# Kernel optimization log

Measured on AMD Instinct MI355X. Metric: run time of the kernel, lower is better.

## Reference

```python
import jax, jax.numpy as jnp
import numpy as np

B, C, H, W = 16, 128, 48, 48
C4 = C // 4
N = H * W
BN_EPS = 1e-5


def conv_bn_relu(x, w, gamma, beta, mean, var):
    # 1x1 conv (no bias) as channel contraction, then eval-mode BatchNorm, then ReLU
    y = jnp.einsum('bchw,oc->bohw', x, w)
    scale = gamma / jnp.sqrt(var + BN_EPS)
    y = y * scale[None, :, None, None] + (beta - mean * scale)[None, :, None, None]
    return jax.nn.relu(y)


def setup_inputs() -> dict:
    key = jax.random.key(0)
    ks = jax.random.split(key, 16)
    inp = {
        'x_en': jax.random.normal(ks[0], (B, C, H, W), dtype=jnp.float32),
        'x_de': jax.random.normal(ks[1], (B, C, H, W), dtype=jnp.float32),
        'x_cat': jax.random.normal(ks[2], (B, 2 * C, H, W), dtype=jnp.float32),
        # Get_KQ: Conv2d(C -> C/4, 1x1, no bias) + BN(C/4) (shared for K and Q)
        'w_kq': jax.random.normal(ks[3], (C4, C), dtype=jnp.float32) * 0.05,
        'kq_gamma': jax.random.normal(ks[4], (C4,), dtype=jnp.float32) * 0.1 + 1.0,
        'kq_beta': jax.random.normal(ks[5], (C4,), dtype=jnp.float32) * 0.1,
        'kq_mean': jax.random.normal(ks[6], (C4,), dtype=jnp.float32) * 0.1,
        'kq_var': jax.random.uniform(ks[7], (C4,), dtype=jnp.float32) + 0.5,
        # Get_V: Conv2d(C -> C, 1x1, no bias) + BN(C)
        'w_v': jax.random.normal(ks[8], (C, C), dtype=jnp.float32) * 0.05,
        'v_gamma': jax.random.normal(ks[9], (C,), dtype=jnp.float32) * 0.1 + 1.0,
        'v_beta': jax.random.normal(ks[10], (C,), dtype=jnp.float32) * 0.1,
        'v_mean': jax.random.normal(ks[11], (C,), dtype=jnp.float32) * 0.1,
        'v_var': jax.random.uniform(ks[12], (C,), dtype=jnp.float32) + 0.5,
        # reduce_channels: Conv2d(2C -> C, 1x1, no bias) + BN(C)
        'w_red': jax.random.normal(ks[13], (C, 2 * C), dtype=jnp.float32) * 0.05,
        'red_gamma': jax.random.normal(ks[14], (C,), dtype=jnp.float32) * 0.1 + 1.0,
        'red_beta': jax.random.normal(ks[15], (C,), dtype=jnp.float32) * 0.1,
        'red_mean': jax.random.normal(jax.random.fold_in(key, 100), (C,), dtype=jnp.float32) * 0.1,
        'red_var': jax.random.uniform(jax.random.fold_in(key, 101), (C,), dtype=jnp.float32) + 0.5,
    }
    return inp


def reference(x_en, x_de, x_cat,
              w_kq, kq_gamma, kq_beta, kq_mean, kq_var,
              w_v, v_gamma, v_beta, v_mean, v_var,
              w_red, red_gamma, red_beta, red_mean, red_var):
    Kf = conv_bn_relu(x_en, w_kq, kq_gamma, kq_beta, kq_mean, kq_var).reshape(B, C4, N)
    Qf = conv_bn_relu(x_de, w_kq, kq_gamma, kq_beta, kq_mean, kq_var).reshape(B, C4, N)
    # KQ[b, n, m] = sum_k K[b, k, n] * Q[b, k, m]  -> [B, N, N]
    KQ = jnp.einsum('bkn,bkm->bnm', Kf, Qf)
    # GLOBAL softmax over the flattened N*N map (per batch), not per row
    A = jax.nn.softmax(KQ.reshape(B, N * N), axis=1).reshape(B, N, N)
    x = conv_bn_relu(x_cat, w_red, red_gamma, red_beta, red_mean, red_var)
    V = conv_bn_relu(x, w_v, v_gamma, v_beta, v_mean, v_var).reshape(B, C, N)
    # FeatureMap[b, c, n] = sum_m V[b, c, m] * A[b, n, m]
    feat = jnp.einsum('bcm,bnm->bcn', V, A).reshape(B, C, H, W)
    return jnp.concatenate([x, feat], axis=1)
```

## Files before the change

### kernel.cpp

```cpp
#include <hip/hip_runtime.h>
#include <math.h>

#define C    128
#define C4   32
#define NN   2304
#define BN_EPS 1e-5f
#define NEG_INF -3.402823466e38f
#define LOG2E 1.4426950408889634f

typedef short bf16x8 __attribute__((ext_vector_type(8)));
typedef float f32x4 __attribute__((ext_vector_type(4)));

#define SOFT_BARRIER() asm volatile("s_waitcnt lgkmcnt(0)\n\ts_barrier" ::: "memory")

__device__ inline unsigned short f2bf(float f) {
    unsigned int u = __float_as_uint(f);
    u += 0x7fffu + ((u >> 16) & 1u);
    return (unsigned short)(u >> 16);
}

__device__ inline unsigned int pk2bf(float a, float b) {
#if __has_builtin(__builtin_amdgcn_cvt_pk_bf16_f32)
    typedef __bf16 bf2 __attribute__((ext_vector_type(2)));
    bf2 v = __builtin_amdgcn_cvt_pk_bf16_f32(a, b);
    return __builtin_bit_cast(unsigned int, v);
#else
    unsigned int ua = __float_as_uint(a); ua += 0x7fffu + ((ua >> 16) & 1u);
    unsigned int ub = __float_as_uint(b); ub += 0x7fffu + ((ub >> 16) & 1u);
    return __builtin_amdgcn_perm(ub, ua, 0x07060302u);
#endif
}

__device__ inline float fexp2(float x) {
#if __has_builtin(__builtin_amdgcn_exp2f)
    return __builtin_amdgcn_exp2f(x);
#else
    return __expf(x * 0.69314718055994531f);
#endif
}


__global__ __launch_bounds__(256) void k_wprep(
    const float* __restrict__ wkq, const float* __restrict__ kq_g,
    const float* __restrict__ kq_b, const float* __restrict__ kq_m,
    const float* __restrict__ kq_v,
    const float* __restrict__ wv, const float* __restrict__ v_g,
    const float* __restrict__ v_b, const float* __restrict__ v_m,
    const float* __restrict__ v_v,
    const float* __restrict__ wred, const float* __restrict__ red_g,
    const float* __restrict__ red_b, const float* __restrict__ red_m,
    const float* __restrict__ red_v,
    unsigned short* __restrict__ wkq_bf, unsigned short* __restrict__ wv_bf,
    unsigned short* __restrict__ wred_bf,
    float* __restrict__ kq_sh, float* __restrict__ v_sh, float* __restrict__ red_sh)
{
    const int t = blockIdx.x * 256 + threadIdx.x;
    if (t < 4096) {
        const int o = t >> 7;
        const float sc = kq_g[o] * rsqrtf(kq_v[o] + BN_EPS);
        wkq_bf[t] = f2bf(wkq[t] * sc);
        if ((t & 127) == 0) kq_sh[o] = kq_b[o] - kq_m[o] * sc;
    } else if (t < 4096 + 16384) {
        const int e = t - 4096;
        const int o = e >> 7;
        const float sc = v_g[o] * rsqrtf(v_v[o] + BN_EPS);
        wv_bf[e] = f2bf(wv[e] * sc);
        if ((e & 127) == 0) v_sh[o] = v_b[o] - v_m[o] * sc;
    } else if (t < 4096 + 16384 + 32768) {
        const int e = t - 20480;
        const int o = e >> 8;
        const float sc = red_g[o] * rsqrtf(red_v[o] + BN_EPS);
        wred_bf[e] = f2bf(wred[e] * sc);
        if ((e & 255) == 0) red_sh[o] = red_b[o] - red_m[o] * sc;
    }
}

__global__ __launch_bounds__(256) void k_kq(
    const float* __restrict__ x0, const float* __restrict__ x1,
    const unsigned short* __restrict__ wbf, const float* __restrict__ shift,
    unsigned short* __restrict__ Kt, unsigned short* __restrict__ Qt)
{
    constexpr int NTILE = 128, R = 8;
    __shared__ unsigned short Xs[NTILE][40];

    const int tid = threadIdx.x;
    const int w = tid >> 6, lane = tid & 63;
    const int quad = lane >> 4, l16 = lane & 15;
    const int b = blockIdx.y, n0 = blockIdx.x * NTILE;
    const int nbase = w * 32;

    const float* xin = (blockIdx.z ? x1 : x0) + (size_t)b * C * NN;
    const int p = tid & 15, g = tid >> 4;

    f32x4 acc[2][2];
#pragma unroll
    for (int mt = 0; mt < 2; mt++)
#pragma unroll
        for (int nt = 0; nt < 2; nt++) acc[mt][nt] = (f32x4){0.f, 0.f, 0.f, 0.f};

    for (int c0 = 0; c0 < C; c0 += 32) {
        __syncthreads();
        {
            const float* xr = xin + (size_t)(c0 + 2 * p) * NN + n0 + g * R;
            float av[R], bv[R];
#pragma unroll
            for (int i4 = 0; i4 < R; i4 += 4) {
                *(float4*)&av[i4] = *(const float4*)&xr[i4];
                *(float4*)&bv[i4] = *(const float4*)&xr[NN + i4];
            }
            unsigned int* Xw = (unsigned int*)Xs;
#pragma unroll
            for (int i = 0; i < R; i++)
                Xw[(g * R + i) * 20 + p] = pk2bf(av[i], bv[i]);
        }
        __syncthreads();
        bf16x8 af[2];
#pragma unroll
        for (int mt = 0; mt < 2; mt++)
            af[mt] = *(const bf16x8*)&wbf[(size_t)(mt * 16 + l16) * C + c0 + quad * 8];
#pragma unroll
        for (int nt = 0; nt < 2; nt++) {
            const bf16x8 bfr = *(const bf16x8*)&Xs[nbase + nt * 16 + l16][quad * 8];
#pragma unroll
            for (int mt = 0; mt < 2; mt++)
                acc[mt][nt] = __builtin_amdgcn_mfma_f32_16x16x32_bf16(af[mt], bfr, acc[mt][nt], 0, 0, 0);
        }
    }

    unsigned short* ob16 = blockIdx.z ? Qt : Kt;
    const float osc = blockIdx.z ? 1.f : LOG2E;
#pragma unroll
    for (int mt = 0; mt < 2; mt++)
#pragma unroll
        for (int nt = 0; nt < 2; nt++)
#pragma unroll
            for (int r = 0; r < 4; r++) {
                const int o = mt * 16 + quad * 4 + r;
                const int n = n0 + nbase + nt * 16 + l16;
                const float sh = shift[o];
                ob16[((size_t)b * NN + n) * 32 + o] =
                    f2bf(fmaxf(acc[mt][nt][r] + sh, 0.f) * osc);
            }
}

__global__ __launch_bounds__(256) void k_redv(
    const float* __restrict__ xcat,
    const unsigned short* __restrict__ wred_bf, const float* __restrict__ red_sh,
    const unsigned short* __restrict__ wv_bf,  const float* __restrict__ v_sh,
    float* __restrict__ out, unsigned short* __restrict__ Vf)
{
    __shared__ unsigned short Xs[64][40];
    __shared__ unsigned int   Xv[64 * 65];

    const int tid = threadIdx.x;
    const int w = tid >> 6, lane = tid & 63;
    const int quad = lane >> 4, l16 = lane & 15;
    const int b = blockIdx.y, n0 = blockIdx.x * 64;
    const float* xin = xcat + (size_t)b * 2 * C * NN;
    const int p = tid & 15, g = tid >> 4;

    f32x4 acc[2][4];
#pragma unroll
    for (int mt = 0; mt < 2; mt++)
#pragma unroll
        for (int nt = 0; nt < 4; nt++) acc[mt][nt] = (f32x4){0.f, 0.f, 0.f, 0.f};

    for (int c0 = 0; c0 < 2 * C; c0 += 32) {
        __syncthreads();
        {
            const float* xr = xin + (size_t)(c0 + 2 * p) * NN + n0 + g * 4;
            float4 av = *(const float4*)&xr[0];
            float4 bv = *(const float4*)&xr[NN];
            unsigned int* Xw = (unsigned int*)Xs;
            Xw[(g * 4 + 0) * 20 + p] = pk2bf(av.x, bv.x);
            Xw[(g * 4 + 1) * 20 + p] = pk2bf(av.y, bv.y);
            Xw[(g * 4 + 2) * 20 + p] = pk2bf(av.z, bv.z);
            Xw[(g * 4 + 3) * 20 + p] = pk2bf(av.w, bv.w);
        }
        __syncthreads();
        bf16x8 af[2];
#pragma unroll
        for (int mt = 0; mt < 2; mt++)
            af[mt] = *(const bf16x8*)&wred_bf[(size_t)(w * 32 + mt * 16 + l16) * (2 * C) + c0 + quad * 8];
#pragma unroll
        for (int nt = 0; nt < 4; nt++) {
            const bf16x8 bfr = *(const bf16x8*)&Xs[nt * 16 + l16][quad * 8];
#pragma unroll
            for (int mt = 0; mt < 2; mt++)
                acc[mt][nt] = __builtin_amdgcn_mfma_f32_16x16x32_bf16(af[mt], bfr, acc[mt][nt], 0, 0, 0);
        }
    }

    {
        float* ob = out + (size_t)b * (2 * C * NN);
#pragma unroll
        for (int mt = 0; mt < 2; mt++) {
            float sh[4];
#pragma unroll
            for (int r = 0; r < 4; r++) sh[r] = red_sh[w * 32 + mt * 16 + quad * 4 + r];
#pragma unroll
            for (int nt = 0; nt < 4; nt++) {
                const int n = n0 + nt * 16 + l16;
                float v[4];
#pragma unroll
                for (int r = 0; r < 4; r++) {
                    const int o = w * 32 + mt * 16 + quad * 4 + r;
                    v[r] = fmaxf(acc[mt][nt][r] + sh[r], 0.f);
                    ob[(size_t)o * NN + n] = v[r];
                }
                const int op0 = 16 * w + mt * 8 + quad * 2;
                Xv[(op0 + 0) * 65 + nt * 16 + l16] = pk2bf(v[0], v[1]);
                Xv[(op0 + 1) * 65 + nt * 16 + l16] = pk2bf(v[2], v[3]);
            }
        }
    }
    SOFT_BARRIER();

    f32x4 vacc[2][4];
#pragma unroll
    for (int mt = 0; mt < 2; mt++)
#pragma unroll
        for (int nt = 0; nt < 4; nt++) vacc[mt][nt] = (f32x4){0.f, 0.f, 0.f, 0.f};

    for (int c0 = 0; c0 < C; c0 += 32) {
        bf16x8 af[2];
#pragma unroll
        for (int mt = 0; mt < 2; mt++)
            af[mt] = *(const bf16x8*)&wv_bf[(size_t)(w * 32 + mt * 16 + l16) * C + c0 + quad * 8];
#pragma unroll
        for (int nt = 0; nt < 4; nt++) {
            const int col = nt * 16 + l16;
            const int cp0 = c0 / 2 + quad * 4;
            uint4 u;
            u.x = Xv[(cp0 + 0) * 65 + col];
            u.y = Xv[(cp0 + 1) * 65 + col];
            u.z = Xv[(cp0 + 2) * 65 + col];
            u.w = Xv[(cp0 + 3) * 65 + col];
            const bf16x8 bfr = __builtin_bit_cast(bf16x8, u);
#pragma unroll
            for (int mt = 0; mt < 2; mt++)
                vacc[mt][nt] = __builtin_amdgcn_mfma_f32_16x16x32_bf16(af[mt], bfr, vacc[mt][nt], 0, 0, 0);
        }
    }

#pragma unroll
    for (int mt = 0; mt < 2; mt++) {
        float sh[4];
#pragma unroll
        for (int r = 0; r < 4; r++) sh[r] = v_sh[w * 32 + mt * 16 + quad * 4 + r];
#pragma unroll
        for (int nt = 0; nt < 4; nt++)
#pragma unroll
            for (int r = 0; r < 4; r++) {
                const int o = w * 32 + mt * 16 + quad * 4 + r;
                const int n = n0 + nt * 16 + l16;
                Vf[((size_t)b * C + o) * NN + n] = f2bf(fmaxf(vacc[mt][nt][r] + sh[r], 0.f));
            }
    }
}

__global__ __launch_bounds__(256) void k_stats(
    const unsigned short* __restrict__ Kt, const unsigned short* __restrict__ Qt,
    float* __restrict__ bmax, float* __restrict__ bsum)
{
    const int tid = threadIdx.x;
    const int w = tid >> 6, lane = tid & 63;
    const int quad = lane >> 4, l16 = lane & 15;
    const int b = blockIdx.z;
    const int n0 = blockIdx.x * 128, m0 = blockIdx.y * 128;
    const unsigned short* Kb = Kt + (size_t)b * NN * 32;
    const unsigned short* Qb = Qt + (size_t)b * NN * 32;

    bf16x8 kf[8], qf[2];
#pragma unroll
    for (int nt = 0; nt < 8; nt++)
        kf[nt] = *(const bf16x8*)&Kb[(size_t)(n0 + nt * 16 + l16) * 32 + quad * 8];
#pragma unroll
    for (int mt = 0; mt < 2; mt++)
        qf[mt] = *(const bf16x8*)&Qb[(size_t)(m0 + w * 32 + mt * 16 + l16) * 32 + quad * 8];

    f32x4 s[16];
#pragma unroll
    for (int mt = 0; mt < 2; mt++)
#pragma unroll
        for (int nt = 0; nt < 8; nt++) {
            f32x4 z = (f32x4){0.f, 0.f, 0.f, 0.f};
            s[mt * 8 + nt] = __builtin_amdgcn_mfma_f32_16x16x32_bf16(qf[mt], kf[nt], z, 0, 0, 0);
        }

    float lmax = NEG_INF;
#pragma unroll
    for (int i = 0; i < 16; i++)
        lmax = fmaxf(lmax, fmaxf(fmaxf(s[i][0], s[i][1]), fmaxf(s[i][2], s[i][3])));
    float lsum = 0.f;
#pragma unroll
    for (int i = 0; i < 16; i++)
        lsum += fexp2(s[i][0] - lmax) + fexp2(s[i][1] - lmax) +
                fexp2(s[i][2] - lmax) + fexp2(s[i][3] - lmax);

#pragma unroll
    for (int off = 32; off > 0; off >>= 1) {
        const float omax = __shfl_xor(lmax, off);
        const float osum = __shfl_xor(lsum, off);
        const float nmax = fmaxf(lmax, omax);
        lsum = lsum * fexp2(lmax - nmax) + osum * fexp2(omax - nmax);
        lmax = nmax;
    }
    __shared__ float smax[4], ssum[4];
    if (lane == 0) { smax[w] = lmax; ssum[w] = lsum; }
    __syncthreads();
    if (tid == 0) {
        float M = smax[0], S = ssum[0];
        for (int i = 1; i < 4; i++) {
            const float nmax = fmaxf(M, smax[i]);
            S = S * fexp2(M - nmax) + ssum[i] * fexp2(smax[i] - nmax);
            M = nmax;
        }
        const int idx = (b * 18 + blockIdx.y) * 18 + blockIdx.x;
        bmax[idx] = M;
        bsum[idx] = S;
    }
}

__global__ __launch_bounds__(256) void k_fin(
    const float* __restrict__ bmax, const float* __restrict__ bsum,
    float* __restrict__ Ms, float* __restrict__ Sinv)
{
    __shared__ float rmax[256], rsum[256];
    const int b = blockIdx.x, tid = threadIdx.x;
    float lmax = NEG_INF, lsum = 0.f;
    for (int i = tid; i < 324; i += 256) {
        const float m = bmax[b * 324 + i], s = bsum[b * 324 + i];
        const float nmax = fmaxf(lmax, m);
        lsum = lsum * fexp2(lmax - nmax) + s * fexp2(m - nmax);
        lmax = nmax;
    }
    rmax[tid] = lmax; rsum[tid] = lsum;
    __syncthreads();
    for (int st = 128; st > 0; st >>= 1) {
        if (tid < st) {
            const float m2 = rmax[tid + st], s2 = rsum[tid + st];
            const float nmax = fmaxf(rmax[tid], m2);
            rsum[tid] = rsum[tid] * fexp2(rmax[tid] - nmax) + s2 * fexp2(m2 - nmax);
            rmax[tid] = nmax;
        }
        __syncthreads();
    }
    if (tid == 0) { Ms[b] = rmax[0]; Sinv[b] = 1.f / rsum[0]; }
}

__global__ __launch_bounds__(256) void k_feat(
    const unsigned short* __restrict__ Kt, const unsigned short* __restrict__ Qt,
    const unsigned short* __restrict__ Vf, const float* __restrict__ Ms,
    const float* __restrict__ Sinv, float* __restrict__ out)
{
    __shared__ __align__(16) unsigned short Et[64][72];
    const int tid = threadIdx.x;
    const int w = tid >> 6, lane = tid & 63;
    const int quad = lane >> 4, l16 = lane & 15;
    const int b = blockIdx.y, n0 = blockIdx.x * 64;
    const unsigned short* Kb = Kt + (size_t)b * NN * 32;
    const unsigned short* Qb = Qt + (size_t)b * NN * 32;
    const unsigned short* Vb = Vf + (size_t)b * C * NN;
    const float M = Ms[b], Si = Sinv[b];

    bf16x8 kf[4];
#pragma unroll
    for (int nt = 0; nt < 4; nt++)
        kf[nt] = *(const bf16x8*)&Kb[(size_t)(n0 + nt * 16 + l16) * 32 + quad * 8];

    f32x4 acc[2][4];
#pragma unroll
    for (int i = 0; i < 2; i++)
#pragma unroll
        for (int j = 0; j < 4; j++) acc[i][j] = (f32x4){0.f, 0.f, 0.f, 0.f};

    bf16x8 qc = *(const bf16x8*)&Qb[(size_t)(w * 16 + l16) * 32 + quad * 8];
    bf16x8 vc[2][2];
#pragma unroll
    for (int ct = 0; ct < 2; ct++)
#pragma unroll
        for (int ks = 0; ks < 2; ks++)
            vc[ct][ks] = *(const bf16x8*)&Vb[(size_t)(w * 32 + ct * 16 + l16) * NN + ks * 32 + quad * 8];

    for (int m0 = 0; m0 < NN; m0 += 64) {
        f32x4 s[4];
#pragma unroll
        for (int nt = 0; nt < 4; nt++) {
            f32x4 z = (f32x4){0.f, 0.f, 0.f, 0.f};
            s[nt] = __builtin_amdgcn_mfma_f32_16x16x32_bf16(qc, kf[nt], z, 0, 0, 0);
        }
        const int m1 = (m0 + 64 < NN) ? m0 + 64 : 0;
        bf16x8 qn = *(const bf16x8*)&Qb[(size_t)(m1 + w * 16 + l16) * 32 + quad * 8];
        bf16x8 vn[2][2];
#pragma unroll
        for (int ct = 0; ct < 2; ct++)
#pragma unroll
            for (int ks = 0; ks < 2; ks++)
                vn[ct][ks] = *(const bf16x8*)&Vb[(size_t)(w * 32 + ct * 16 + l16) * NN + m1 + ks * 32 + quad * 8];

#pragma unroll
        for (int nt = 0; nt < 4; nt++) {
            const unsigned int u0 = pk2bf(fexp2(s[nt][0] - M), fexp2(s[nt][1] - M));
            const unsigned int u1 = pk2bf(fexp2(s[nt][2] - M), fexp2(s[nt][3] - M));
            *(uint2*)&Et[nt * 16 + l16][w * 16 + quad * 4] = make_uint2(u0, u1);
        }
        SOFT_BARRIER();
#pragma unroll
        for (int ks = 0; ks < 2; ks++) {
#pragma unroll
            for (int nt = 0; nt < 4; nt++) {
                const bf16x8 ef = *(const bf16x8*)&Et[nt * 16 + l16][ks * 32 + quad * 8];
                acc[0][nt] = __builtin_amdgcn_mfma_f32_16x16x32_bf16(vc[0][ks], ef, acc[0][nt], 0, 0, 0);
                acc[1][nt] = __builtin_amdgcn_mfma_f32_16x16x32_bf16(vc[1][ks], ef, acc[1][nt], 0, 0, 0);
            }
        }
        SOFT_BARRIER();
        qc = qn;
#pragma unroll
        for (int ct = 0; ct < 2; ct++)
#pragma unroll
            for (int ks = 0; ks < 2; ks++) vc[ct][ks] = vn[ct][ks];
    }

    float* ob = out + (size_t)b * 2 * C * NN + (size_t)C * NN + n0;
#pragma unroll
    for (int ct = 0; ct < 2; ct++)
#pragma unroll
        for (int nt = 0; nt < 4; nt++)
#pragma unroll
            for (int r = 0; r < 4; r++) {
                const int c = w * 32 + ct * 16 + quad * 4 + r;
                ob[(size_t)c * NN + nt * 16 + l16] = acc[ct][nt][r] * Si;
            }
}

extern "C" void kernel_launch(void* const* d_in, const int* in_sizes, int n_in,
                              void* d_out, int out_size, void* d_ws, size_t ws_size,
                              hipStream_t stream)
{
    const float* x_en   = (const float*)d_in[0];
    const float* x_de   = (const float*)d_in[1];
    const float* x_cat  = (const float*)d_in[2];
    const float* w_kq   = (const float*)d_in[3];
    const float* kq_g   = (const float*)d_in[4];
    const float* kq_b   = (const float*)d_in[5];
    const float* kq_m   = (const float*)d_in[6];
    const float* kq_v   = (const float*)d_in[7];
    const float* w_v    = (const float*)d_in[8];
    const float* v_g    = (const float*)d_in[9];
    const float* v_b    = (const float*)d_in[10];
    const float* v_m    = (const float*)d_in[11];
    const float* v_v    = (const float*)d_in[12];
    const float* w_red  = (const float*)d_in[13];
    const float* red_g  = (const float*)d_in[14];
    const float* red_b  = (const float*)d_in[15];
    const float* red_m  = (const float*)d_in[16];
    const float* red_v  = (const float*)d_in[17];

    unsigned short* Kt      = (unsigned short*)d_ws;
    unsigned short* Qt      = Kt + 1179648;
    unsigned short* Vf      = Qt + 1179648;
    unsigned short* wkq_bf  = Vf + 4718592;
    unsigned short* wv_bf   = wkq_bf + 4096;
    unsigned short* wred_bf = wv_bf + 16384;
    float* bmax = (float*)(wred_bf + 32768);
    float* bsum = bmax + 16 * 324;
    float* Ms   = bsum + 16 * 324;
    float* Sinv = Ms + 16;
    float* kq_sh  = Sinv + 16;
    float* v_sh   = kq_sh + 32;
    float* red_sh = v_sh + 128;
    float* out  = (float*)d_out;

    k_wprep<<<208, 256, 0, stream>>>(
        w_kq, kq_g, kq_b, kq_m, kq_v,
        w_v, v_g, v_b, v_m, v_v,
        w_red, red_g, red_b, red_m, red_v,
        wkq_bf, wv_bf, wred_bf, kq_sh, v_sh, red_sh);

    k_kq  <<<dim3(18, 16, 2), 256, 0, stream>>>(x_en, x_de, wkq_bf, kq_sh, Kt, Qt);
    k_redv<<<dim3(36, 16), 256, 0, stream>>>(x_cat, wred_bf, red_sh, wv_bf, v_sh, out, Vf);

    k_stats<<<dim3(18, 18, 16), 256, 0, stream>>>(Kt, Qt, bmax, bsum);
    k_fin  <<<16, 256, 0, stream>>>(bmax, bsum, Ms, Sinv);
    k_feat <<<dim3(36, 16), 256, 0, stream>>>(Kt, Qt, Vf, Ms, Sinv, out);
}
```

Baseline: 251.0 us.

## Fuse softmax stats into feature pass with online per-column max and split-M

Removes the separate stats pass that recomputed all KQ scores, and computes an online per-column running max and sum inside the feature kernel instead. The M range is split in two halves (grid z=2) to double parallelism. Partial results are stored (split 0 in fp32 to the output, split 1 in bf16 to scratch). A finalize kernel computes the global max and per-column rescale factors, and an elementwise kernel combines the two partials. This trades the redundant QK^T compute for extra rescale work per iteration, an extra barrier-dependent cross-wave max, and a memory round-trip of the partial outputs.

```diff
diff --git a/kernel.cpp b/kernel.cpp
--- a/kernel.cpp
+++ b/kernel.cpp
@@ -259,81 +259,175 @@
     }
 }
 
-__global__ __launch_bounds__(256) void k_stats(
+__global__ __launch_bounds__(256) void k_feat(
     const unsigned short* __restrict__ Kt, const unsigned short* __restrict__ Qt,
-    float* __restrict__ bmax, float* __restrict__ bsum)
-{
+    const unsigned short* __restrict__ Vf, float* __restrict__ out,
+    unsigned short* __restrict__ Dp, float* __restrict__ Mn, float* __restrict__ Sn)
+{
+    __shared__ __align__(16) unsigned short Et[64][72];
+    __shared__ float cmax[4][64];
     const int tid = threadIdx.x;
     const int w = tid >> 6, lane = tid & 63;
     const int quad = lane >> 4, l16 = lane & 15;
-    const int b = blockIdx.z;
-    const int n0 = blockIdx.x * 128, m0 = blockIdx.y * 128;
+    const int b = blockIdx.y, n0 = blockIdx.x * 64, split = blockIdx.z;
+    const int mlo = split * (NN / 2), mhi = mlo + NN / 2;
     const unsigned short* Kb = Kt + (size_t)b * NN * 32;
     const unsigned short* Qb = Qt + (size_t)b * NN * 32;
-
-    bf16x8 kf[8], qf[2];
-#pragma unroll
-    for (int nt = 0; nt < 8; nt++)
+    const unsigned short* Vb = Vf + (size_t)b * C * NN;
+
+    bf16x8 kf[4];
+#pragma unroll
+    for (int nt = 0; nt < 4; nt++)
         kf[nt] = *(const bf16x8*)&Kb[(size_t)(n0 + nt * 16 + l16) * 32 + quad * 8];
-#pragma unroll
-    for (int mt = 0; mt < 2; mt++)
-        qf[mt] = *(const bf16x8*)&Qb[(size_t)(m0 + w * 32 + mt * 16 + l16) * 32 + quad * 8];
-
-    f32x4 s[16];
-#pragma unroll
-    for (int mt = 0; mt < 2; mt++)
-#pragma unroll
-        for (int nt = 0; nt < 8; nt++) {
+
+    f32x4 acc[2][4];
+#pragma unroll
+    for (int i = 0; i < 2; i++)
+#pragma unroll
+        for (int j = 0; j < 4; j++) acc[i][j] = (f32x4){0.f, 0.f, 0.f, 0.f};
+    float Mcol[4], Scol[4];
+#pragma unroll
+    for (int nt = 0; nt < 4; nt++) { Mcol[nt] = NEG_INF; Scol[nt] = 0.f; }
+
+    bf16x8 qc = *(const bf16x8*)&Qb[(size_t)(mlo + w * 16 + l16) * 32 + quad * 8];
+    bf16x8 vc[2][2];
+#pragma unroll
+    for (int ct = 0; ct < 2; ct++)
+#pragma unroll
+        for (int ks = 0; ks < 2; ks++)
+            vc[ct][ks] = *(const bf16x8*)&Vb[(size_t)(w * 32 + ct * 16 + l16) * NN + mlo + ks * 32 + quad * 8];
+
+    for (int m0 = mlo; m0 < mhi; m0 += 64) {
+        f32x4 s[4];
+#pragma unroll
+        for (int nt = 0; nt < 4; nt++) {
             f32x4 z = (f32x4){0.f, 0.f, 0.f, 0.f};
-            s[mt * 8 + nt] = __builtin_amdgcn_mfma_f32_16x16x32_bf16(qf[mt], kf[nt], z, 0, 0, 0);
-        }
-
-    float lmax = NEG_INF;
-#pragma unroll
-    for (int i = 0; i < 16; i++)
-        lmax = fmaxf(lmax, fmaxf(fmaxf(s[i][0], s[i][1]), fmaxf(s[i][2], s[i][3])));
-    float lsum = 0.f;
-#pragma unroll
-    for (int i = 0; i < 16; i++)
-        lsum += fexp2(s[i][0] - lmax) + fexp2(s[i][1] - lmax) +
-                fexp2(s[i][2] - lmax) + fexp2(s[i][3] - lmax);
-
-#pragma unroll
-    for (int off = 32; off > 0; off >>= 1) {
-        const float omax = __shfl_xor(lmax, off);
-        const float osum = __shfl_xor(lsum, off);
-        const float nmax = fmaxf(lmax, omax);
-        lsum = lsum * fexp2(lmax - nmax) + osum * fexp2(omax - nmax);
-        lmax = nmax;
-    }
-    __shared__ float smax[4], ssum[4];
-    if (lane == 0) { smax[w] = lmax; ssum[w] = lsum; }
-    __syncthreads();
-    if (tid == 0) {
-        float M = smax[0], S = ssum[0];
-        for (int i = 1; i < 4; i++) {
-            const float nmax = fmaxf(M, smax[i]);
-            S = S * fexp2(M - nmax) + ssum[i] * fexp2(smax[i] - nmax);
-            M = nmax;
-        }
-        const int idx = (b * 18 + blockIdx.y) * 18 + blockIdx.x;
-        bmax[idx] = M;
-        bsum[idx] = S;
-    }
-}
-
-__global__ __launch_bounds__(256) void k_fin(
-    const float* __restrict__ bmax, const float* __restrict__ bsum,
-    float* __restrict__ Ms, float* __restrict__ Sinv)
+            s[nt] = __builtin_amdgcn_mfma_f32_16x16x32_bf16(qc, kf[nt], z, 0, 0, 0);
+        }
+        const int m1 = (m0 + 64 < mhi) ? m0 + 64 : mlo;
+        bf16x8 qn = *(const bf16x8*)&Qb[(size_t)(m1 + w * 16 + l16) * 32 + quad * 8];
+        bf16x8 vn[2][2];
+#pragma unroll
+        for (int ct = 0; ct < 2; ct++)
+#pragma unroll
+            for (int ks = 0; ks < 2; ks++)
+                vn[ct][ks] = *(const bf16x8*)&Vb[(size_t)(w * 32 + ct * 16 + l16) * NN + m1 + ks * 32 + quad * 8];
+
+        float cm[4];
+#pragma unroll
+        for (int nt = 0; nt < 4; nt++) {
+            cm[nt] = fmaxf(fmaxf(s[nt][0], s[nt][1]), fmaxf(s[nt][2], s[nt][3]));
+            cm[nt] = fmaxf(cm[nt], __shfl_xor(cm[nt], 16));
+            cm[nt] = fmaxf(cm[nt], __shfl_xor(cm[nt], 32));
+        }
+        if (lane < 16) {
+#pragma unroll
+            for (int nt = 0; nt < 4; nt++) cmax[w][nt * 16 + lane] = cm[nt];
+        }
+        SOFT_BARRIER();
+        float scale[4];
+#pragma unroll
+        for (int nt = 0; nt < 4; nt++) {
+            const int col = nt * 16 + l16;
+            const float m4 = fmaxf(fmaxf(cmax[0][col], cmax[1][col]),
+                                   fmaxf(cmax[2][col], cmax[3][col]));
+            const float newM = fmaxf(Mcol[nt], m4);
+            scale[nt] = fexp2(Mcol[nt] - newM);
+            Mcol[nt] = newM;
+        }
+#pragma unroll
+        for (int nt = 0; nt < 4; nt++) {
+            acc[0][nt] *= scale[nt];
+            acc[1][nt] *= scale[nt];
+            const float e0 = fexp2(s[nt][0] - Mcol[nt]);
+            const float e1 = fexp2(s[nt][1] - Mcol[nt]);
+            const float e2 = fexp2(s[nt][2] - Mcol[nt]);
+            const float e3 = fexp2(s[nt][3] - Mcol[nt]);
+            Scol[nt] = Scol[nt] * scale[nt] + ((e0 + e1) + (e2 + e3));
+            *(uint2*)&Et[nt * 16 + l16][w * 16 + quad * 4] =
+                make_uint2(pk2bf(e0, e1), pk2bf(e2, e3));
+        }
+        SOFT_BARRIER();
+#pragma unroll
+        for (int ks = 0; ks < 2; ks++) {
+#pragma unroll
+            for (int nt = 0; nt < 4; nt++) {
+                const bf16x8 ef = *(const bf16x8*)&Et[nt * 16 + l16][ks * 32 + quad * 8];
+                acc[0][nt] = __builtin_amdgcn_mfma_f32_16x16x32_bf16(vc[0][ks], ef, acc[0][nt], 0, 0, 0);
+                acc[1][nt] = __builtin_amdgcn_mfma_f32_16x16x32_bf16(vc[1][ks], ef, acc[1][nt], 0, 0, 0);
+            }
+        }
+        qc = qn;
+#pragma unroll
+        for (int ct = 0; ct < 2; ct++)
+#pragma unroll
+            for (int ks = 0; ks < 2; ks++) vc[ct][ks] = vn[ct][ks];
+    }
+
+#pragma unroll
+    for (int nt = 0; nt < 4; nt++) {
+        Scol[nt] += __shfl_xor(Scol[nt], 16);
+        Scol[nt] += __shfl_xor(Scol[nt], 32);
+    }
+    SOFT_BARRIER();
+    if (lane < 16) {
+#pragma unroll
+        for (int nt = 0; nt < 4; nt++) cmax[w][nt * 16 + lane] = Scol[nt];
+    }
+    SOFT_BARRIER();
+    if (w == 0 && lane < 16) {
+        float* Mb = Mn + ((size_t)split * 16 + b) * NN + n0;
+        float* Sb = Sn + ((size_t)split * 16 + b) * NN + n0;
+#pragma unroll
+        for (int nt = 0; nt < 4; nt++) {
+            const int col = nt * 16 + lane;
+            Mb[col] = Mcol[nt];
+            Sb[col] = cmax[0][col] + cmax[1][col] + cmax[2][col] + cmax[3][col];
+        }
+    }
+
+    if (split == 0) {
+        float* ob = out + (size_t)b * 2 * C * NN + (size_t)C * NN + n0;
+#pragma unroll
+        for (int ct = 0; ct < 2; ct++)
+#pragma unroll
+            for (int nt = 0; nt < 4; nt++)
+#pragma unroll
+                for (int r = 0; r < 4; r++) {
+                    const int c = w * 32 + ct * 16 + quad * 4 + r;
+                    ob[(size_t)c * NN + nt * 16 + l16] = acc[ct][nt][r];
+                }
+    } else {
+        unsigned short* db = Dp + (size_t)b * C * NN + n0;
+#pragma unroll
+        for (int ct = 0; ct < 2; ct++)
+#pragma unroll
+            for (int nt = 0; nt < 4; nt++)
+#pragma unroll
+                for (int r = 0; r < 4; r++) {
+                    const int c = w * 32 + ct * 16 + quad * 4 + r;
+                    db[(size_t)c * NN + nt * 16 + l16] = f2bf(acc[ct][nt][r]);
+                }
+    }
+}
+
+__global__ __launch_bounds__(256) void k_fin2(
+    const float* __restrict__ Mn, const float* __restrict__ Sn,
+    float* __restrict__ cs)
 {
     __shared__ float rmax[256], rsum[256];
     const int b = blockIdx.x, tid = threadIdx.x;
     float lmax = NEG_INF, lsum = 0.f;
-    for (int i = tid; i < 324; i += 256) {
-        const float m = bmax[b * 324 + i], s = bsum[b * 324 + i];
-        const float nmax = fmaxf(lmax, m);
-        lsum = lsum * fexp2(lmax - nmax) + s * fexp2(m - nmax);
-        lmax = nmax;
+#pragma unroll
+    for (int s = 0; s < 2; s++) {
+        const float* Mb = Mn + ((size_t)s * 16 + b) * NN;
+        const float* Sb = Sn + ((size_t)s * 16 + b) * NN;
+        for (int i = tid; i < NN; i += 256) {
+            const float m = Mb[i], sv = Sb[i];
+            const float nmax = fmaxf(lmax, m);
+            lsum = lsum * fexp2(lmax - nmax) + sv * fexp2(m - nmax);
+            lmax = nmax;
+        }
     }
     rmax[tid] = lmax; rsum[tid] = lsum;
     __syncthreads();
@@ -346,93 +440,38 @@
         }
         __syncthreads();
     }
-    if (tid == 0) { Ms[b] = rmax[0]; Sinv[b] = 1.f / rsum[0]; }
-}
-
-__global__ __launch_bounds__(256) void k_feat(
-    const unsigned short* __restrict__ Kt, const unsigned short* __restrict__ Qt,
-    const unsigned short* __restrict__ Vf, const float* __restrict__ Ms,
-    const float* __restrict__ Sinv, float* __restrict__ out)
-{
-    __shared__ __align__(16) unsigned short Et[64][72];
-    const int tid = threadIdx.x;
-    const int w = tid >> 6, lane = tid & 63;
-    const int quad = lane >> 4, l16 = lane & 15;
-    const int b = blockIdx.y, n0 = blockIdx.x * 64;
-    const unsigned short* Kb = Kt + (size_t)b * NN * 32;
-    const unsigned short* Qb = Qt + (size_t)b * NN * 32;
-    const unsigned short* Vb = Vf + (size_t)b * C * NN;
-    const float M = Ms[b], Si = Sinv[b];
-
-    bf16x8 kf[4];
-#pragma unroll
-    for (int nt = 0; nt < 4; nt++)
-        kf[nt] = *(const bf16x8*)&Kb[(size_t)(n0 + nt * 16 + l16) * 32 + quad * 8];
-
-    f32x4 acc[2][4];
-#pragma unroll
-    for (int i = 0; i < 2; i++)
-#pragma unroll
-        for (int j = 0; j < 4; j++) acc[i][j] = (f32x4){0.f, 0.f, 0.f, 0.f};
-
-    bf16x8 qc = *(const bf16x8*)&Qb[(size_t)(w * 16 + l16) * 32 + quad * 8];
-    bf16x8 vc[2][2];
-#pragma unroll
-    for (int ct = 0; ct < 2; ct++)
-#pragma unroll
-        for (int ks = 0; ks < 2; ks++)
-            vc[ct][ks] = *(const bf16x8*)&Vb[(size_t)(w * 32 + ct * 16 + l16) * NN + ks * 32 + quad * 8];
-
-    for (int m0 = 0; m0 < NN; m0 += 64) {
-        f32x4 s[4];
-#pragma unroll
-        for (int nt = 0; nt < 4; nt++) {
-            f32x4 z = (f32x4){0.f, 0.f, 0.f, 0.f};
-            s[nt] = __builtin_amdgcn_mfma_f32_16x16x32_bf16(qc, kf[nt], z, 0, 0, 0);
-        }
-        const int m1 = (m0 + 64 < NN) ? m0 + 64 : 0;
-        bf16x8 qn = *(const bf16x8*)&Qb[(size_t)(m1 + w * 16 + l16) * 32 + quad * 8];
-        bf16x8 vn[2][2];
-#pragma unroll
-        for (int ct = 0; ct < 2; ct++)
-#pragma unroll
-            for (int ks = 0; ks < 2; ks++)
-                vn[ct][ks] = *(const bf16x8*)&Vb[(size_t)(w * 32 + ct * 16 + l16) * NN + m1 + ks * 32 + quad * 8];
-
-#pragma unroll
-        for (int nt = 0; nt < 4; nt++) {
-            const unsigned int u0 = pk2bf(fexp2(s[nt][0] - M), fexp2(s[nt][1] - M));
-            const unsigned int u1 = pk2bf(fexp2(s[nt][2] - M), fexp2(s[nt][3] - M));
-            *(uint2*)&Et[nt * 16 + l16][w * 16 + quad * 4] = make_uint2(u0, u1);
-        }
-        SOFT_BARRIER();
-#pragma unroll
-        for (int ks = 0; ks < 2; ks++) {
-#pragma unroll
-            for (int nt = 0; nt < 4; nt++) {
-                const bf16x8 ef = *(const bf16x8*)&Et[nt * 16 + l16][ks * 32 + quad * 8];
-                acc[0][nt] = __builtin_amdgcn_mfma_f32_16x16x32_bf16(vc[0][ks], ef, acc[0][nt], 0, 0, 0);
-                acc[1][nt] = __builtin_amdgcn_mfma_f32_16x16x32_bf16(vc[1][ks], ef, acc[1][nt], 0, 0, 0);
-            }
-        }
-        SOFT_BARRIER();
-        qc = qn;
-#pragma unroll
-        for (int ct = 0; ct < 2; ct++)
-#pragma unroll
-            for (int ks = 0; ks < 2; ks++) vc[ct][ks] = vn[ct][ks];
-    }
-
-    float* ob = out + (size_t)b * 2 * C * NN + (size_t)C * NN + n0;
-#pragma unroll
-    for (int ct = 0; ct < 2; ct++)
-#pragma unroll
-        for (int nt = 0; nt < 4; nt++)
-#pragma unroll
-            for (int r = 0; r < 4; r++) {
-                const int c = w * 32 + ct * 16 + quad * 4 + r;
-                ob[(size_t)c * NN + nt * 16 + l16] = acc[ct][nt][r] * Si;
-            }
+    const float Mg = rmax[0];
+    const float rS = 1.f / rsum[0];
+#pragma unroll
+    for (int s = 0; s < 2; s++) {
+        const float* Mb = Mn + ((size_t)s * 16 + b) * NN;
+        float* cb = cs + ((size_t)s * 16 + b) * NN;
+        for (int i = tid; i < NN; i += 256)
+            cb[i] = fexp2(Mb[i] - Mg) * rS;
+    }
+}
+
+__global__ __launch_bounds__(256) void k_scale(
+    float* __restrict__ out, const unsigned short* __restrict__ Dp,
+    const float* __restrict__ cs)
+{
+    const size_t e = ((size_t)blockIdx.x * 256 + threadIdx.x) * 4;
+    const int b = (int)(e / (C * NN));
+    const int r = (int)(e % (C * NN));
+    const int c = r / NN, n = r % NN;
+
+    float* op = out + (size_t)b * 2 * C * NN + (size_t)(C + c) * NN + n;
+    float4 d0 = *(const float4*)op;
+    const ushort4 d1u = *(const ushort4*)&Dp[((size_t)b * C + c) * NN + n];
+    const float4 f0 = *(const float4*)&cs[(size_t)b * NN + n];
+    const float4 f1 = *(const float4*)&cs[(size_t)(16 + b) * NN + n];
+
+    float4 o;
+    o.x = d0.x * f0.x + __uint_as_float((unsigned int)d1u.x << 16) * f1.x;
+    o.y = d0.y * f0.y + __uint_as_float((unsigned int)d1u.y << 16) * f1.y;
+    o.z = d0.z * f0.z + __uint_as_float((unsigned int)d1u.z << 16) * f1.z;
+    o.w = d0.w * f0.w + __uint_as_float((unsigned int)d1u.w << 16) * f1.w;
+    *(float4*)op = o;
 }
 
 extern "C" void kernel_launch(void* const* d_in, const int* in_sizes, int n_in,
@@ -464,11 +503,11 @@
     unsigned short* wkq_bf  = Vf + 4718592;
     unsigned short* wv_bf   = wkq_bf + 4096;
     unsigned short* wred_bf = wv_bf + 16384;
-    float* bmax = (float*)(wred_bf + 32768);
-    float* bsum = bmax + 16 * 324;
-    float* Ms   = bsum + 16 * 324;
-    float* Sinv = Ms + 16;
-    float* kq_sh  = Sinv + 16;
+    unsigned short* Dp      = wred_bf + 32768;
+    float* Mn   = (float*)(Dp + 4718592);
+    float* Sn   = Mn + 2 * 16 * NN;
+    float* cs   = Sn + 2 * 16 * NN;
+    float* kq_sh  = cs + 2 * 16 * NN;
     float* v_sh   = kq_sh + 32;
     float* red_sh = v_sh + 128;
     float* out  = (float*)d_out;
@@ -482,7 +521,7 @@
     k_kq  <<<dim3(18, 16, 2), 256, 0, stream>>>(x_en, x_de, wkq_bf, kq_sh, Kt, Qt);
     k_redv<<<dim3(36, 16), 256, 0, stream>>>(x_cat, wred_bf, red_sh, wv_bf, v_sh, out, Vf);
 
-    k_stats<<<dim3(18, 18, 16), 256, 0, stream>>>(Kt, Qt, bmax, bsum);
-    k_fin  <<<16, 256, 0, stream>>>(bmax, bsum, Ms, Sinv);
-    k_feat <<<dim3(36, 16), 256, 0, stream>>>(Kt, Qt, Vf, Ms, Sinv, out);
-}
+    k_feat <<<dim3(36, 16, 2), 256, 0, stream>>>(Kt, Qt, Vf, out, Dp, Mn, Sn);
+    k_fin2 <<<16, 256, 0, stream>>>(Mn, Sn, cs);
+    k_scale<<<4608, 256, 0, stream>>>(out, Dp, cs);
+}
```

Result: slower. 256.8 us (+2.3%).
